# Kernel optimization log

Measured on AMD Instinct MI355X. Metric: run time of the kernel, lower is better.

## Reference

```python
import jax, jax.numpy as jnp
import numpy as np

D_MODEL = 768
D_STATE = 64
EXPAND = 2
D_INNER = EXPAND * D_MODEL
B, L = 2, 1024


def setup_inputs() -> dict:
    key = jax.random.key(0)
    ks = jax.random.split(key, 12)
    def xavier(k, shape):
        fan_in, fan_out = shape[0], shape[1]
        a = np.sqrt(6.0 / (fan_in + fan_out)).astype(np.float32)
        return jax.random.uniform(k, shape, jnp.float32, -a, a)
    x = jax.random.normal(ks[0], (B, L, D_MODEL), jnp.float32)
    W_in = xavier(ks[1], (D_MODEL, 2 * D_INNER))
    W_x = xavier(ks[2], (D_INNER, 2 * D_STATE + D_INNER))
    W_dt = xavier(ks[3], (D_STATE, D_INNER))
    b_dt = jax.random.uniform(ks[4], (D_INNER,), jnp.float32, -0.1, 0.1)
    A_log = jax.random.uniform(ks[5], (D_INNER, D_STATE), jnp.float32, -4.0, -1.0)
    Dp = 1.0 + 0.1 * jax.random.normal(ks[6], (D_INNER,), jnp.float32)
    W_out = xavier(ks[7], (D_INNER, D_MODEL))
    ln_g = jnp.ones((D_MODEL,), jnp.float32)
    ln_b = jnp.zeros((D_MODEL,), jnp.float32)
    return {"x": x, "W_in": W_in, "W_x": W_x, "W_dt": W_dt, "b_dt": b_dt,
            "A_log": A_log, "Dp": Dp, "W_out": W_out, "ln_g": ln_g, "ln_b": ln_b}


def _s6_forward(x, W_in, W_x, W_dt, b_dt, A_log, Dp, W_out, ln_g, ln_b):
    residual = x
    xr = x @ W_in                                    # (B,L,2*d_inner)
    xs, res = xr[..., :D_INNER], xr[..., D_INNER:]
    xs = jax.nn.silu(xs)
    # selective scan parameters
    x_dbl = xs @ W_x                                 # (B,L,2*d_state+d_inner)
    B_sel = x_dbl[..., :D_STATE]                     # (B,L,d_state)
    delta_in = x_dbl[..., D_STATE:2 * D_STATE]       # (B,L,d_state)
    C_sel = x_dbl[..., 2 * D_STATE:]                 # (B,L,d_inner)
    delta = jax.nn.softplus(delta_in @ W_dt + b_dt)  # (B,L,d_inner)
    delta = jnp.minimum(delta, 10.0)
    A = -jnp.exp(A_log.astype(jnp.float32))          # (d_inner,d_state)

    def step(h, inp):
        x_t, d_t, B_t, C_t = inp                     # (B,di) (B,di) (B,ds) (B,di)
        dA = jnp.exp(d_t[:, :, None] * A[None])      # (B,di,ds)
        dB = d_t[:, :, None] * B_t[:, None, :]       # (B,di,ds)
        h = dA * h + dB * x_t[:, :, None]
        y_t = C_t * jnp.sum(h, axis=-1)              # (B,di): sum(C[...,None]*h,-1)
        return h, y_t

    h0 = jnp.zeros((x.shape[0], D_INNER, D_STATE), xs.dtype)
    time_major = lambda a: jnp.swapaxes(a, 0, 1)
    _, ys = jax.lax.scan(step, h0, (time_major(xs), time_major(delta),
                                    time_major(B_sel), time_major(C_sel)))
    y = jnp.swapaxes(ys, 0, 1)                       # (B,L,d_inner)
    y = y + xs * Dp
    y = y * jax.nn.silu(res)
    out = y @ W_out + residual
    mu = jnp.mean(out, axis=-1, keepdims=True)
    var = jnp.var(out, axis=-1, keepdims=True)
    return (out - mu) * jax.lax.rsqrt(var + 1e-5) * ln_g + ln_b


def reference(x, W_in, W_x, W_dt, b_dt, A_log, Dp, W_out, ln_g, ln_b):
    return _s6_forward(x, W_in, W_x, W_dt, b_dt, A_log, Dp, W_out, ln_g, ln_b)
```

## Files before the change

### kernel.cpp

```cpp
#include <hip/hip_runtime.h>

typedef __bf16 bf16x8 __attribute__((ext_vector_type(8)));
typedef short short8 __attribute__((ext_vector_type(8)));
typedef float f32x4 __attribute__((ext_vector_type(4)));
typedef float f32x2 __attribute__((ext_vector_type(2)));
typedef unsigned short ushort_t;

__device__ __forceinline__ ushort_t f2bf(float f) {
  union { float f; unsigned u; } v; v.f = f;
  unsigned r = v.u + 0x7fffu + ((v.u >> 16) & 1u);
  return (ushort_t)(r >> 16);
}
__device__ __forceinline__ float bf2f(ushort_t u) {
  return __int_as_float(((unsigned)u) << 16);
}

__device__ __forceinline__ void g2lds16(const void* g, void* l) {
  __builtin_amdgcn_global_load_lds(
      (const __attribute__((address_space(1))) void*)g,
      (__attribute__((address_space(3))) void*)l, 16, 0, 0);
}

__device__ __forceinline__ float rlane(float v, int l) {
  return __int_as_float(__builtin_amdgcn_readlane(__float_as_int(v), l));
}

__device__ __forceinline__ float fexp2(float x) {
#if __has_builtin(__builtin_amdgcn_exp2f)
  return __builtin_amdgcn_exp2f(x);
#else
  return exp2f(x);
#endif
}

__device__ __forceinline__ f32x2 pk_fma(f32x2 a, f32x2 b, f32x2 c) {
#if __has_builtin(__builtin_elementwise_fma)
  return __builtin_elementwise_fma(a, b, c);
#else
  return (f32x2){fmaf(a.x, b.x, c.x), fmaf(a.y, b.y, c.y)};
#endif
}

template<int CTRL>
__device__ __forceinline__ float dpp_step(float x) {
  int t = __builtin_amdgcn_update_dpp(0, __float_as_int(x), CTRL, 0xf, 0xf, false);
  return x + __int_as_float(t);
}
__device__ __forceinline__ float wave_sum64(float v) {
  v = dpp_step<0x111>(v);
  v = dpp_step<0x112>(v);
  v = dpp_step<0x114>(v);
  v = dpp_step<0x118>(v);
  v = dpp_step<0x142>(v);
  v = dpp_step<0x143>(v);
  return v;
}
__device__ __forceinline__ float row_sum16(float v) {
  v = dpp_step<0x111>(v);
  v = dpp_step<0x112>(v);
  v = dpp_step<0x114>(v);
  v = dpp_step<0x118>(v);
  return v;
}
__device__ __forceinline__ float bcast_row15(float v) {
  return __int_as_float(__builtin_amdgcn_ds_swizzle(__float_as_int(v), 0x1F0));
}

__global__ __launch_bounds__(256)
void prep_kernel(const float* __restrict__ x, ushort_t* __restrict__ xbf,
                 const float* __restrict__ W_in, ushort_t* __restrict__ WinT,
                 const float* __restrict__ W_x, ushort_t* __restrict__ WxT,
                 const float* __restrict__ W_out, ushort_t* __restrict__ WoutT) {
  __shared__ float tile[32][33];
  const int r = blockIdx.x, tid = threadIdx.x;
  if (r < 1536) {
    int i = (r * 256 + tid) * 4;
    float4 v = *(const float4*)(x + i);
    union { ushort_t u[4]; uint2 v2; } o;
    o.u[0] = f2bf(v.x); o.u[1] = f2bf(v.y); o.u[2] = f2bf(v.z); o.u[3] = f2bf(v.w);
    *(uint2*)(xbf + i) = o.v2;
    return;
  }
  const float* W; ushort_t* Wt; int K, N, bx, by;
  if (r < 3840)      { int rr = r - 1536; W = W_in;  Wt = WinT;  K = 768;  N = 3072; bx = rr % 96; by = rr / 96; }
  else if (r < 6336) { int rr = r - 3840; W = W_x;   Wt = WxT;   K = 1536; N = 1664; bx = rr % 52; by = rr / 52; }
  else               { int rr = r - 6336; W = W_out; Wt = WoutT; K = 1536; N = 768;  bx = rr % 24; by = rr / 24; }
  const int n0 = bx * 32, k0 = by * 32;
  const int tx = tid & 31, ty = tid >> 5;
#pragma unroll
  for (int rr = 0; rr < 32; rr += 8)
    tile[ty + rr][tx] = W[(size_t)(k0 + ty + rr) * N + n0 + tx];
  __syncthreads();
#pragma unroll
  for (int rr = 0; rr < 32; rr += 8)
    Wt[(size_t)(n0 + ty + rr) * K + k0 + tx] = f2bf(tile[tx][ty + rr]);
}

template<int MODE>
__global__ __launch_bounds__(256)
void gemm_bf16(const ushort_t* __restrict__ A, const ushort_t* __restrict__ Bt,
               const int K, const int lda, const int ldb,
               float* __restrict__ out0, ushort_t* __restrict__ out1,
               float* __restrict__ out2, const float* __restrict__ resid) {
  __shared__ __align__(16) ushort_t Asl[128 * 32];
  __shared__ __align__(16) ushort_t Bsl[128 * 32];
  const int tid = threadIdx.x;
  const int lane = tid & 63;
  const int wid = tid >> 6;
  const int wm = wid >> 1, wn = wid & 1;
  const int lr = lane & 15, lk = lane >> 4;
  const int bm = blockIdx.y, bn = blockIdx.x;
  if (MODE == 2) {
    const int z = blockIdx.z;
    A += z * 384;
    Bt += z * 384;
    out0 += (size_t)z * 2048 * 768;
  }
  const ushort_t* Ab = A + (size_t)bm * 128 * lda;
  const ushort_t* Bb = Bt + (size_t)bn * 128 * ldb;

  f32x4 acc[4][4];
#pragma unroll
  for (int i = 0; i < 4; ++i)
#pragma unroll
    for (int j = 0; j < 4; ++j) acc[i][j] = (f32x4){0.f, 0.f, 0.f, 0.f};

  for (int k0 = 0; k0 < K; k0 += 32) {
#pragma unroll
    for (int it = 0; it < 2; ++it) {
      const int cb = ((it << 2) + wid) << 6;
      const int ch = cb + lane;
      const int row = ch >> 2;
      const int c8 = (ch & 3) << 3;
      g2lds16(Ab + (size_t)row * lda + k0 + c8, Asl + (size_t)cb * 8);
      g2lds16(Bb + (size_t)row * ldb + k0 + c8, Bsl + (size_t)cb * 8);
    }
    __syncthreads();
    short8 av[4], bv[4];
#pragma unroll
    for (int i = 0; i < 4; ++i)
      av[i] = *(const short8*)(Asl + ((wm * 64 + i * 16 + lr) * 32 + lk * 8));
#pragma unroll
    for (int j = 0; j < 4; ++j)
      bv[j] = *(const short8*)(Bsl + ((wn * 64 + j * 16 + lr) * 32 + lk * 8));
#pragma unroll
    for (int i = 0; i < 4; ++i)
#pragma unroll
      for (int j = 0; j < 4; ++j)
        acc[i][j] = __builtin_amdgcn_mfma_f32_16x16x32_bf16(
            __builtin_bit_cast(bf16x8, av[i]), __builtin_bit_cast(bf16x8, bv[j]),
            acc[i][j], 0, 0, 0);
    __syncthreads();
  }

  const int mb = bm * 128 + wm * 64 + (lane >> 4) * 4;
  const int nb = bn * 128 + wn * 64 + (lane & 15);
#pragma unroll
  for (int i = 0; i < 4; ++i) {
#pragma unroll
    for (int j = 0; j < 4; ++j) {
      const int n = nb + j * 16;
#pragma unroll
      for (int r = 0; r < 4; ++r) {
        const int m = mb + i * 16 + r;
        float v = acc[i][j][r];
        if (MODE == 0) {
          float sv = v / (1.f + __expf(-v));
          if (n < 1536) {
            out0[(size_t)m * 1536 + n] = sv;
            out1[(size_t)m * 1536 + n] = f2bf(sv);
          } else {
            out2[(size_t)m * 1536 + (n - 1536)] = sv;
          }
        } else if (MODE == 1) {
          out0[(size_t)m * 1664 + n] = v;
        } else {
          out0[(size_t)m * 768 + n] = v;
        }
      }
    }
  }
}

__global__ __launch_bounds__(256)
void dt_gemm(const float* __restrict__ xdbl, const float* __restrict__ Wdt,
             const float* __restrict__ bdt, float* __restrict__ delta) {
  __shared__ float Wl[64][256];
  __shared__ float Xl[32][64];
  const int tid = threadIdx.x;
  const int n0 = blockIdx.x << 8;
  const int m0 = blockIdx.y << 5;
  for (int i = tid; i < 64 * 256; i += 256) {
    int k = i >> 8, nn = i & 255;
    Wl[k][nn] = Wdt[(size_t)k * 1536 + n0 + nn];
  }
  for (int i = tid; i < 32 * 64; i += 256) {
    int mm = i >> 6, k = i & 63;
    Xl[mm][k] = xdbl[(size_t)(m0 + mm) * 1664 + 64 + k];
  }
  __syncthreads();
  float bv = bdt[n0 + tid];
  for (int mm = 0; mm < 32; ++mm) {
    float acc = bv;
#pragma unroll
    for (int k = 0; k < 64; ++k) acc = fmaf(Xl[mm][k], Wl[k][tid], acc);
    float sp = fmaxf(acc, 0.f) + log1pf(__expf(-fabsf(acc)));
    delta[(size_t)(m0 + mm) * 1536 + n0 + tid] = fminf(sp, 10.f);
  }
}


__global__ __launch_bounds__(256)
void scan_pass1(const float* __restrict__ xdbl, const float* __restrict__ delta,
                const float* __restrict__ xs, const float* __restrict__ A_log,
                float* __restrict__ Qb, float* __restrict__ Dsum) {
  __shared__ __align__(16) ushort_t Btl[64 * 64];
  __shared__ __align__(16) f32x2 dtdx[64][16];
  const int tid = threadIdx.x;
  const int lane = tid & 63;
  const int wid = tid >> 6;
  const int i16 = lane & 15;
  const int ch = wid * 4 + (lane >> 4);
  const int seg = blockIdx.x, b = blockIdx.z;
  const int d0 = blockIdx.y * 16;
  const int d = d0 + ch;
  const int t0 = seg << 6;
  const size_t r0 = (size_t)b * 1024;

#pragma unroll
  for (int i = 0; i < 4; ++i) {
    int q = i * 256 + tid;
    int t = q >> 4, s0 = (q & 15) << 2;
    float4 v = *(const float4*)(xdbl + (r0 + t0 + t) * 1664 + s0);
    ushort4 u;
    u.x = f2bf(v.x); u.y = f2bf(v.y); u.z = f2bf(v.z); u.w = f2bf(v.w);
    *(ushort4*)&Btl[t * 64 + s0] = u;
  }
  float dtg[4];
#pragma unroll
  for (int c = 0; c < 4; ++c) {
    int dc = d0 + wid * 4 + c;
    dtg[c] = delta[(r0 + t0 + lane) * 1536 + dc];
    float dxg = dtg[c] * xs[(r0 + t0 + lane) * 1536 + dc];
    dtdx[lane][(wid * 4 + c) ^ i16] = (f32x2){dtg[c], dxg};
  }
  float ds0 = rlane(wave_sum64(dtg[0]), 63);
  float ds1 = rlane(wave_sum64(dtg[1]), 63);
  float ds2 = rlane(wave_sum64(dtg[2]), 63);
  float ds3 = rlane(wave_sum64(dtg[3]), 63);
  if (lane == 0) {
    const size_t sb0 = (size_t)(b * 16 + seg) * 1536 + d0 + wid * 4;
    *(float4*)(Dsum + sb0) = make_float4(ds0, ds1, ds2, ds3);
  }

  float4 Av = *(const float4*)(A_log + (size_t)d * 64 + i16 * 4);
  const f32x2 A01 = {-__expf(Av.x) * 1.44269504f, -__expf(Av.y) * 1.44269504f};
  const f32x2 A23 = {-__expf(Av.z) * 1.44269504f, -__expf(Av.w) * 1.44269504f};

  __syncthreads();

  const char* dtb = (const char*)&dtdx[0][0];
  const char* Bb8 = (const char*)Btl + (i16 << 3);
  const int chb = ch << 3;
  f32x2 h01 = {0.f, 0.f}, h23 = {0.f, 0.f};
#pragma unroll
  for (int tt = 0; tt < 64; ++tt) {
    f32x2 dd = *(const f32x2*)(dtb + tt * 128 + (chb ^ ((tt & 15) << 3)));
    uint2 ub = *(const uint2*)(Bb8 + tt * 128);
    f32x2 b01 = {__int_as_float(ub.x << 16), __int_as_float(ub.x & 0xFFFF0000u)};
    f32x2 b23 = {__int_as_float(ub.y << 16), __int_as_float(ub.y & 0xFFFF0000u)};
    f32x2 dt2 = {dd.x, dd.x}, dx2 = {dd.y, dd.y};
    f32x2 m01 = dt2 * A01, m23 = dt2 * A23;
    f32x2 e01 = {fexp2(m01.x), fexp2(m01.y)};
    f32x2 e23 = {fexp2(m23.x), fexp2(m23.y)};
    h01 = pk_fma(e01, h01, dx2 * b01);
    h23 = pk_fma(e23, h23, dx2 * b23);
  }
  const size_t sb = (size_t)(b * 16 + seg) * 1536 + d;
  *(float4*)(Qb + sb * 64 + i16 * 4) = make_float4(h01.x, h01.y, h23.x, h23.y);
}

__global__ __launch_bounds__(256)
void scan_combine(float* __restrict__ Qb, const float* __restrict__ Dsum,
                  const float* __restrict__ A_log) {
  const int tid = threadIdx.x;
  const int lane = tid & 63;
  const int wave = blockIdx.x * 4 + (tid >> 6);
  const int bb = (wave >= 1536) ? 1 : 0;
  const int d = wave - bb * 1536;
  const float Aval2 = -__expf(A_log[(size_t)d * 64 + lane]) * 1.44269504f;
  float qv[16], Pv[16];
#pragma unroll
  for (int j = 0; j < 16; ++j) {
    const size_t sb = ((size_t)(bb * 16 + j) * 1536 + d);
    qv[j] = Qb[sb * 64 + lane];
    Pv[j] = fexp2(Aval2 * Dsum[sb]);
  }
  float h = 0.f;
#pragma unroll
  for (int j = 0; j < 16; ++j) {
    const size_t sb = ((size_t)(bb * 16 + j) * 1536 + d);
    Qb[sb * 64 + lane] = h;
    h = fmaf(Pv[j], h, qv[j]);
  }
}

__global__ __launch_bounds__(256)
void scan_pass2(const float* __restrict__ xdbl, const float* __restrict__ delta,
                const float* __restrict__ xs, const float* __restrict__ sres,
                const float* __restrict__ A_log, const float* __restrict__ Dp,
                const float* __restrict__ Qb, ushort_t* __restrict__ ybf) {
  __shared__ __align__(16) ushort_t Btl[64 * 64];
  __shared__ __align__(16) f32x2 dtdx[64][16];
  __shared__ __align__(16) float ytmp[64][16];
  const int tid = threadIdx.x;
  const int lane = tid & 63;
  const int wid = tid >> 6;
  const int i16 = lane & 15;
  const int ch = wid * 4 + (lane >> 4);
  const int seg = blockIdx.x, b = blockIdx.z;
  const int d0 = blockIdx.y * 16;
  const int d = d0 + ch;
  const int t0 = seg << 6;
  const size_t r0 = (size_t)b * 1024;

#pragma unroll
  for (int i = 0; i < 4; ++i) {
    int q = i * 256 + tid;
    int t = q >> 4, s0 = (q & 15) << 2;
    float4 v = *(const float4*)(xdbl + (r0 + t0 + t) * 1664 + s0);
    ushort4 u;
    u.x = f2bf(v.x); u.y = f2bf(v.y); u.z = f2bf(v.z); u.w = f2bf(v.w);
    *(ushort4*)&Btl[t * 64 + s0] = u;
  }
#pragma unroll
  for (int c = 0; c < 4; ++c) {
    int dc = d0 + wid * 4 + c;
    float dt = delta[(r0 + t0 + lane) * 1536 + dc];
    float dx = dt * xs[(r0 + t0 + lane) * 1536 + dc];
    dtdx[lane][(wid * 4 + c) ^ i16] = (f32x2){dt, dx};
  }

  float4 Av = *(const float4*)(A_log + (size_t)d * 64 + i16 * 4);
  const f32x2 A01 = {-__expf(Av.x) * 1.44269504f, -__expf(Av.y) * 1.44269504f};
  const f32x2 A23 = {-__expf(Av.z) * 1.44269504f, -__expf(Av.w) * 1.44269504f};
  const size_t sb = (size_t)(b * 16 + seg) * 1536 + d;
  float4 hq = *(const float4*)(Qb + sb * 64 + i16 * 4);
  f32x2 h01 = {hq.x, hq.y}, h23 = {hq.z, hq.w};

  __syncthreads();

  const char* dtb = (const char*)&dtdx[0][0];
  const char* Bb8 = (const char*)Btl + (i16 << 3);
  const int chb = ch << 3;
  float acc0 = 0.f, acc1 = 0.f, acc2 = 0.f, acc3 = 0.f;
#pragma unroll
  for (int tt = 0; tt < 64; ++tt) {
    f32x2 dd = *(const f32x2*)(dtb + tt * 128 + (chb ^ ((tt & 15) << 3)));
    uint2 ub = *(const uint2*)(Bb8 + tt * 128);
    f32x2 b01 = {__int_as_float(ub.x << 16), __int_as_float(ub.x & 0xFFFF0000u)};
    f32x2 b23 = {__int_as_float(ub.y << 16), __int_as_float(ub.y & 0xFFFF0000u)};
    f32x2 dt2 = {dd.x, dd.x}, dx2 = {dd.y, dd.y};
    f32x2 m01 = dt2 * A01, m23 = dt2 * A23;
    f32x2 e01 = {fexp2(m01.x), fexp2(m01.y)};
    f32x2 e23 = {fexp2(m23.x), fexp2(m23.y)};
    h01 = pk_fma(e01, h01, dx2 * b01);
    h23 = pk_fma(e23, h23, dx2 * b23);
    f32x2 hs = h01 + h23;
    float s4 = hs.x + hs.y;
    float Sv = bcast_row15(row_sum16(s4));
    bool m = (i16 == (tt & 15));
    if ((tt >> 4) == 0) acc0 = m ? Sv : acc0;
    else if ((tt >> 4) == 1) acc1 = m ? Sv : acc1;
    else if ((tt >> 4) == 2) acc2 = m ? Sv : acc2;
    else acc3 = m ? Sv : acc3;
  }

  ytmp[0 * 16 + i16][ch] = acc0;
  ytmp[1 * 16 + i16][ch] = acc1;
  ytmp[2 * 16 + i16][ch] = acc2;
  ytmp[3 * 16 + i16][ch] = acc3;
  __syncthreads();

  const int ch2 = tid & 15;
  const int tr = tid >> 4;
  const float dp2 = Dp[d0 + ch2];
#pragma unroll
  for (int r2 = 0; r2 < 4; ++r2) {
    const int t = tr + (r2 << 4);
    const size_t gi = r0 + t0 + t;
    float yv = ytmp[t][ch2];
    float Ct = xdbl[gi * 1664 + 128 + d0 + ch2];
    float xt = xs[gi * 1536 + d0 + ch2];
    float rt = sres[gi * 1536 + d0 + ch2];
    ybf[gi * 1536 + d0 + ch2] = f2bf((Ct * yv + xt * dp2) * rt);
  }
}

__global__ __launch_bounds__(256)
void ln_kernel(const float* __restrict__ part, const float* __restrict__ x,
               const float* __restrict__ g, const float* __restrict__ be,
               float* __restrict__ outp) {
  const int row = blockIdx.x, tid = threadIdx.x;
  const size_t ro = (size_t)row * 768;
  const float* p0 = part + ro;
  const float* p1 = part + 1572864 + ro;
  const float* p2 = part + 3145728 + ro;
  const float* p3 = part + 4718592 + ro;
  const float* xr = x + ro;
  float v0 = p0[tid] + p1[tid] + p2[tid] + p3[tid] + xr[tid];
  float v1 = p0[tid + 256] + p1[tid + 256] + p2[tid + 256] + p3[tid + 256] + xr[tid + 256];
  float v2 = p0[tid + 512] + p1[tid + 512] + p2[tid + 512] + p3[tid + 512] + xr[tid + 512];
  __shared__ float sb[4];
  const int wid = tid >> 6;
  float s = wave_sum64(v0 + v1 + v2);
  if ((tid & 63) == 63) sb[wid] = s;
  __syncthreads();
  float mu = (sb[0] + sb[1] + sb[2] + sb[3]) * (1.f / 768.f);
  __syncthreads();
  float d0 = v0 - mu, d1 = v1 - mu, d2 = v2 - mu;
  float q = wave_sum64(d0 * d0 + d1 * d1 + d2 * d2);
  if ((tid & 63) == 63) sb[wid] = q;
  __syncthreads();
  float var = (sb[0] + sb[1] + sb[2] + sb[3]) * (1.f / 768.f);
  float inv = rsqrtf(var + 1e-5f);
  float* po = outp + ro;
  po[tid]       = d0 * inv * g[tid]       + be[tid];
  po[tid + 256] = d1 * inv * g[tid + 256] + be[tid + 256];
  po[tid + 512] = d2 * inv * g[tid + 512] + be[tid + 512];
}

extern "C" void kernel_launch(void* const* d_in, const int* in_sizes, int n_in,
                              void* d_out, int out_size, void* d_ws, size_t ws_size,
                              hipStream_t stream) {
  (void)in_sizes; (void)n_in; (void)out_size; (void)ws_size;
  const float* x     = (const float*)d_in[0];
  const float* W_in  = (const float*)d_in[1];
  const float* W_x   = (const float*)d_in[2];
  const float* W_dt  = (const float*)d_in[3];
  const float* b_dt  = (const float*)d_in[4];
  const float* A_log = (const float*)d_in[5];
  const float* Dp    = (const float*)d_in[6];
  const float* W_out = (const float*)d_in[7];
  const float* ln_g  = (const float*)d_in[8];
  const float* ln_b  = (const float*)d_in[9];
  float* out = (float*)d_out;
  char* ws = (char*)d_ws;

  ushort_t* xbf   = (ushort_t*)(ws + 0);
  ushort_t* WinT  = (ushort_t*)(ws + 3145728);
  ushort_t* WxT   = (ushort_t*)(ws + 7864320);
  ushort_t* WoutT = (ushort_t*)(ws + 12976128);
  float*    xs_f  = (float*)   (ws + 15335424);
  ushort_t* xs_bf = (ushort_t*)(ws + 27918336);
  float*    sresp = (float*)   (ws + 34209792);
  float*    xdbl  = (float*)   (ws + 46792704);
  float*    dlt   = (float*)   (ws + 60424192);
  ushort_t* ybf   = (ushort_t*)(ws + 73007104);
  float*    Qbuf  = (float*)   (ws + 0);
  float*    Dsum  = (float*)   (ws + 12582912);
  float*    part  = (float*)   (ws + 15335424);

  prep_kernel<<<7488, 256, 0, stream>>>(x, xbf, W_in, WinT, W_x, WxT, W_out, WoutT);

  gemm_bf16<0><<<dim3(24, 16), 256, 0, stream>>>(xbf, WinT, 768, 768, 768,
                                                 xs_f, xs_bf, sresp, nullptr);
  gemm_bf16<1><<<dim3(13, 16), 256, 0, stream>>>(xs_bf, WxT, 1536, 1536, 1536,
                                                 xdbl, nullptr, nullptr, nullptr);
  dt_gemm<<<dim3(6, 64), 256, 0, stream>>>(xdbl, W_dt, b_dt, dlt);

  scan_pass1<<<dim3(16, 96, 2), 256, 0, stream>>>(xdbl, dlt, xs_f, A_log, Qbuf, Dsum);
  scan_combine<<<768, 256, 0, stream>>>(Qbuf, Dsum, A_log);
  scan_pass2<<<dim3(16, 96, 2), 256, 0, stream>>>(xdbl, dlt, xs_f, sresp, A_log, Dp, Qbuf, ybf);

  gemm_bf16<2><<<dim3(6, 16, 4), 256, 0, stream>>>(ybf, WoutT, 384, 1536, 1536,
                                                   part, nullptr, nullptr, nullptr);
  ln_kernel<<<2048, 256, 0, stream>>>(part, x, ln_g, ln_b, out);
}
```

Baseline: 215.4 us.

## Pair timesteps in scan LDS layout and write row sums directly per lane

```diff
diff --git a/kernel.cpp b/kernel.cpp
--- a/kernel.cpp
+++ b/kernel.cpp
@@ -10,9 +10,6 @@
   union { float f; unsigned u; } v; v.f = f;
   unsigned r = v.u + 0x7fffu + ((v.u >> 16) & 1u);
   return (ushort_t)(r >> 16);
-}
-__device__ __forceinline__ float bf2f(ushort_t u) {
-  return __int_as_float(((unsigned)u) << 16);
 }
 
 __device__ __forceinline__ void g2lds16(const void* g, void* l) {
@@ -61,9 +58,6 @@
   v = dpp_step<0x114>(v);
   v = dpp_step<0x118>(v);
   return v;
-}
-__device__ __forceinline__ float bcast_row15(float v) {
-  return __int_as_float(__builtin_amdgcn_ds_swizzle(__float_as_int(v), 0x1F0));
 }
 
 __global__ __launch_bounds__(256)
@@ -214,8 +208,8 @@
 void scan_pass1(const float* __restrict__ xdbl, const float* __restrict__ delta,
                 const float* __restrict__ xs, const float* __restrict__ A_log,
                 float* __restrict__ Qb, float* __restrict__ Dsum) {
-  __shared__ __align__(16) ushort_t Btl[64 * 64];
-  __shared__ __align__(16) f32x2 dtdx[64][16];
+  __shared__ __align__(16) ushort_t Btl[32 * 64 * 2];
+  __shared__ __align__(16) f32x4 ddl[32 * 16];
   const int tid = threadIdx.x;
   const int lane = tid & 63;
   const int wid = tid >> 6;
@@ -228,21 +222,29 @@
   const size_t r0 = (size_t)b * 1024;
 
 #pragma unroll
-  for (int i = 0; i < 4; ++i) {
+  for (int i = 0; i < 2; ++i) {
     int q = i * 256 + tid;
-    int t = q >> 4, s0 = (q & 15) << 2;
-    float4 v = *(const float4*)(xdbl + (r0 + t0 + t) * 1664 + s0);
-    ushort4 u;
-    u.x = f2bf(v.x); u.y = f2bf(v.y); u.z = f2bf(v.z); u.w = f2bf(v.w);
-    *(ushort4*)&Btl[t * 64 + s0] = u;
-  }
+    int t2 = q >> 4, s0 = (q & 15) << 2;
+    const float* rowE = xdbl + (r0 + t0 + 2 * t2) * 1664 + s0;
+    float4 ve = *(const float4*)rowE;
+    float4 vo = *(const float4*)(rowE + 1664);
+    uint4 u;
+    u.x = f2bf(ve.x) | ((unsigned)f2bf(vo.x) << 16);
+    u.y = f2bf(ve.y) | ((unsigned)f2bf(vo.y) << 16);
+    u.z = f2bf(ve.z) | ((unsigned)f2bf(vo.z) << 16);
+    u.w = f2bf(ve.w) | ((unsigned)f2bf(vo.w) << 16);
+    *(uint4*)&Btl[(t2 * 64 + s0) * 2] = u;
+  }
+  const int t2w = lane >> 1;
   float dtg[4];
 #pragma unroll
   for (int c = 0; c < 4; ++c) {
     int dc = d0 + wid * 4 + c;
     dtg[c] = delta[(r0 + t0 + lane) * 1536 + dc];
     float dxg = dtg[c] * xs[(r0 + t0 + lane) * 1536 + dc];
-    dtdx[lane][(wid * 4 + c) ^ i16] = (f32x2){dtg[c], dxg};
+    int cx = (wid * 4 + c) ^ (t2w & 15);
+    float* slot = (float*)&ddl[t2w * 16 + cx] + (lane & 1) * 2;
+    *(f32x2*)slot = (f32x2){dtg[c], dxg};
   }
   float ds0 = rlane(wave_sum64(dtg[0]), 63);
   float ds1 = rlane(wave_sum64(dtg[1]), 63);
@@ -259,22 +261,26 @@
 
   __syncthreads();
 
-  const char* dtb = (const char*)&dtdx[0][0];
-  const char* Bb8 = (const char*)Btl + (i16 << 3);
-  const int chb = ch << 3;
+  const char* ddb = (const char*)ddl;
+  const char* Bb8 = (const char*)Btl + (i16 << 4);
+  const int chb = ch << 4;
   f32x2 h01 = {0.f, 0.f}, h23 = {0.f, 0.f};
 #pragma unroll
-  for (int tt = 0; tt < 64; ++tt) {
-    f32x2 dd = *(const f32x2*)(dtb + tt * 128 + (chb ^ ((tt & 15) << 3)));
-    uint2 ub = *(const uint2*)(Bb8 + tt * 128);
-    f32x2 b01 = {__int_as_float(ub.x << 16), __int_as_float(ub.x & 0xFFFF0000u)};
-    f32x2 b23 = {__int_as_float(ub.y << 16), __int_as_float(ub.y & 0xFFFF0000u)};
+  for (int t2 = 0; t2 < 32; ++t2) {
+    f32x4 dd = *(const f32x4*)(ddb + t2 * 256 + (chb ^ ((t2 & 15) << 4)));
+    uint4 ub = *(const uint4*)(Bb8 + t2 * 256);
+    f32x2 b01 = {__int_as_float(ub.x << 16), __int_as_float(ub.y << 16)};
+    f32x2 b23 = {__int_as_float(ub.z << 16), __int_as_float(ub.w << 16)};
     f32x2 dt2 = {dd.x, dd.x}, dx2 = {dd.y, dd.y};
     f32x2 m01 = dt2 * A01, m23 = dt2 * A23;
-    f32x2 e01 = {fexp2(m01.x), fexp2(m01.y)};
-    f32x2 e23 = {fexp2(m23.x), fexp2(m23.y)};
-    h01 = pk_fma(e01, h01, dx2 * b01);
-    h23 = pk_fma(e23, h23, dx2 * b23);
+    h01 = pk_fma((f32x2){fexp2(m01.x), fexp2(m01.y)}, h01, dx2 * b01);
+    h23 = pk_fma((f32x2){fexp2(m23.x), fexp2(m23.y)}, h23, dx2 * b23);
+    b01 = (f32x2){__int_as_float(ub.x & 0xFFFF0000u), __int_as_float(ub.y & 0xFFFF0000u)};
+    b23 = (f32x2){__int_as_float(ub.z & 0xFFFF0000u), __int_as_float(ub.w & 0xFFFF0000u)};
+    dt2 = (f32x2){dd.z, dd.z}; dx2 = (f32x2){dd.w, dd.w};
+    m01 = dt2 * A01; m23 = dt2 * A23;
+    h01 = pk_fma((f32x2){fexp2(m01.x), fexp2(m01.y)}, h01, dx2 * b01);
+    h23 = pk_fma((f32x2){fexp2(m23.x), fexp2(m23.y)}, h23, dx2 * b23);
   }
   const size_t sb = (size_t)(b * 16 + seg) * 1536 + d;
   *(float4*)(Qb + sb * 64 + i16 * 4) = make_float4(h01.x, h01.y, h23.x, h23.y);
@@ -310,9 +316,9 @@
                 const float* __restrict__ xs, const float* __restrict__ sres,
                 const float* __restrict__ A_log, const float* __restrict__ Dp,
                 const float* __restrict__ Qb, ushort_t* __restrict__ ybf) {
-  __shared__ __align__(16) ushort_t Btl[64 * 64];
-  __shared__ __align__(16) f32x2 dtdx[64][16];
-  __shared__ __align__(16) float ytmp[64][16];
+  __shared__ __align__(16) ushort_t Btl[32 * 64 * 2];
+  __shared__ __align__(16) f32x4 ddl[32 * 16];
+  __shared__ __align__(16) f32x2 ytl[32 * 16];
   const int tid = threadIdx.x;
   const int lane = tid & 63;
   const int wid = tid >> 6;
@@ -325,20 +331,28 @@
   const size_t r0 = (size_t)b * 1024;
 
 #pragma unroll
-  for (int i = 0; i < 4; ++i) {
+  for (int i = 0; i < 2; ++i) {
     int q = i * 256 + tid;
-    int t = q >> 4, s0 = (q & 15) << 2;
-    float4 v = *(const float4*)(xdbl + (r0 + t0 + t) * 1664 + s0);
-    ushort4 u;
-    u.x = f2bf(v.x); u.y = f2bf(v.y); u.z = f2bf(v.z); u.w = f2bf(v.w);
-    *(ushort4*)&Btl[t * 64 + s0] = u;
-  }
+    int t2 = q >> 4, s0 = (q & 15) << 2;
+    const float* rowE = xdbl + (r0 + t0 + 2 * t2) * 1664 + s0;
+    float4 ve = *(const float4*)rowE;
+    float4 vo = *(const float4*)(rowE + 1664);
+    uint4 u;
+    u.x = f2bf(ve.x) | ((unsigned)f2bf(vo.x) << 16);
+    u.y = f2bf(ve.y) | ((unsigned)f2bf(vo.y) << 16);
+    u.z = f2bf(ve.z) | ((unsigned)f2bf(vo.z) << 16);
+    u.w = f2bf(ve.w) | ((unsigned)f2bf(vo.w) << 16);
+    *(uint4*)&Btl[(t2 * 64 + s0) * 2] = u;
+  }
+  const int t2w = lane >> 1;
 #pragma unroll
   for (int c = 0; c < 4; ++c) {
     int dc = d0 + wid * 4 + c;
     float dt = delta[(r0 + t0 + lane) * 1536 + dc];
     float dx = dt * xs[(r0 + t0 + lane) * 1536 + dc];
-    dtdx[lane][(wid * 4 + c) ^ i16] = (f32x2){dt, dx};
+    int cx = (wid * 4 + c) ^ (t2w & 15);
+    float* slot = (float*)&ddl[t2w * 16 + cx] + (lane & 1) * 2;
+    *(f32x2*)slot = (f32x2){dt, dx};
   }
 
   float4 Av = *(const float4*)(A_log + (size_t)d * 64 + i16 * 4);
@@ -350,46 +364,43 @@
 
   __syncthreads();
 
-  const char* dtb = (const char*)&dtdx[0][0];
-  const char* Bb8 = (const char*)Btl + (i16 << 3);
-  const int chb = ch << 3;
-  float acc0 = 0.f, acc1 = 0.f, acc2 = 0.f, acc3 = 0.f;
-#pragma unroll
-  for (int tt = 0; tt < 64; ++tt) {
-    f32x2 dd = *(const f32x2*)(dtb + tt * 128 + (chb ^ ((tt & 15) << 3)));
-    uint2 ub = *(const uint2*)(Bb8 + tt * 128);
-    f32x2 b01 = {__int_as_float(ub.x << 16), __int_as_float(ub.x & 0xFFFF0000u)};
-    f32x2 b23 = {__int_as_float(ub.y << 16), __int_as_float(ub.y & 0xFFFF0000u)};
+  const char* ddb = (const char*)ddl;
+  const char* Bb8 = (const char*)Btl + (i16 << 4);
+  const int chb = ch << 4;
+  const bool wlane = (i16 == 15);
+#pragma unroll
+  for (int t2 = 0; t2 < 32; ++t2) {
+    f32x4 dd = *(const f32x4*)(ddb + t2 * 256 + (chb ^ ((t2 & 15) << 4)));
+    uint4 ub = *(const uint4*)(Bb8 + t2 * 256);
+    f32x2 b01 = {__int_as_float(ub.x << 16), __int_as_float(ub.y << 16)};
+    f32x2 b23 = {__int_as_float(ub.z << 16), __int_as_float(ub.w << 16)};
     f32x2 dt2 = {dd.x, dd.x}, dx2 = {dd.y, dd.y};
     f32x2 m01 = dt2 * A01, m23 = dt2 * A23;
-    f32x2 e01 = {fexp2(m01.x), fexp2(m01.y)};
-    f32x2 e23 = {fexp2(m23.x), fexp2(m23.y)};
-    h01 = pk_fma(e01, h01, dx2 * b01);
-    h23 = pk_fma(e23, h23, dx2 * b23);
-    f32x2 hs = h01 + h23;
-    float s4 = hs.x + hs.y;
-    float Sv = bcast_row15(row_sum16(s4));
-    bool m = (i16 == (tt & 15));
-    if ((tt >> 4) == 0) acc0 = m ? Sv : acc0;
-    else if ((tt >> 4) == 1) acc1 = m ? Sv : acc1;
-    else if ((tt >> 4) == 2) acc2 = m ? Sv : acc2;
-    else acc3 = m ? Sv : acc3;
-  }
-
-  ytmp[0 * 16 + i16][ch] = acc0;
-  ytmp[1 * 16 + i16][ch] = acc1;
-  ytmp[2 * 16 + i16][ch] = acc2;
-  ytmp[3 * 16 + i16][ch] = acc3;
+    h01 = pk_fma((f32x2){fexp2(m01.x), fexp2(m01.y)}, h01, dx2 * b01);
+    h23 = pk_fma((f32x2){fexp2(m23.x), fexp2(m23.y)}, h23, dx2 * b23);
+    f32x2 hsE = h01 + h23;
+    float WE = row_sum16(hsE.x + hsE.y);
+    b01 = (f32x2){__int_as_float(ub.x & 0xFFFF0000u), __int_as_float(ub.y & 0xFFFF0000u)};
+    b23 = (f32x2){__int_as_float(ub.z & 0xFFFF0000u), __int_as_float(ub.w & 0xFFFF0000u)};
+    dt2 = (f32x2){dd.z, dd.z}; dx2 = (f32x2){dd.w, dd.w};
+    m01 = dt2 * A01; m23 = dt2 * A23;
+    h01 = pk_fma((f32x2){fexp2(m01.x), fexp2(m01.y)}, h01, dx2 * b01);
+    h23 = pk_fma((f32x2){fexp2(m23.x), fexp2(m23.y)}, h23, dx2 * b23);
+    f32x2 hsO = h01 + h23;
+    float WO = row_sum16(hsO.x + hsO.y);
+    if (wlane) ytl[t2 * 16 + ch] = (f32x2){WE, WO};
+  }
   __syncthreads();
 
   const int ch2 = tid & 15;
   const int tr = tid >> 4;
   const float dp2 = Dp[d0 + ch2];
+  const float* ytf = (const float*)ytl;
 #pragma unroll
   for (int r2 = 0; r2 < 4; ++r2) {
     const int t = tr + (r2 << 4);
     const size_t gi = r0 + t0 + t;
-    float yv = ytmp[t][ch2];
+    float yv = ytf[(t >> 1) * 32 + ch2 * 2 + (t & 1)];
     float Ct = xdbl[gi * 1664 + 128 + d0 + ch2];
     float xt = xs[gi * 1536 + d0 + ch2];
     float rt = sres[gi * 1536 + d0 + ch2];
```

New measurement: 219.0 us. About the same (+1.7%).
